# Optimization experiments

Hardware: AMD Instinct MI355X
Metric: run time of the kernel (lower is better)

Reference implementation:

```python
import jax, jax.numpy as jnp
import numpy as np
from jax import lax

EPS = 1e-5
K = 7
G = 4


def _dwconv_bn(x, w, g, b, m, v):
    # depthwise 3x3, pad 1, then BN (eval mode with running stats)
    C = x.shape[1]
    y = lax.conv_general_dilated(x, w, (1, 1), [(1, 1), (1, 1)],
                                 feature_group_count=C,
                                 dimension_numbers=('NCHW', 'OIHW', 'NCHW'))
    scale = (g / jnp.sqrt(v + EPS))[None, :, None, None]
    return (y - m[None, :, None, None]) * scale + b[None, :, None, None]


def _proj(t, pw1, pb1, pw2, pb2):
    # 1x1 conv -> GELU(exact) -> 1x1 conv, on small spatial maps
    h = jnp.einsum('bchw,oc->bohw', t, pw1) + pb1[None, :, None, None]
    h = jax.nn.gelu(h, approximate=False)
    return jnp.einsum('bchw,oc->bohw', h, pw2) + pb2[None, :, None, None]


def setup_inputs() -> dict:
    key = jax.random.key(0)
    ks = jax.random.split(key, 17)
    B, C, H, W = 16, 256, 56, 56
    r = C // 4
    inp = {
        'x1': jax.random.normal(ks[0], (B, C, H, W), jnp.float32),
        'dw1_w': jax.random.normal(ks[1], (C, 1, 3, 3), jnp.float32) * 0.1,
        'dw1_g': jax.random.uniform(ks[2], (C,), jnp.float32, 0.5, 1.5),
        'dw1_b': jax.random.normal(ks[3], (C,), jnp.float32) * 0.1,
        'dw1_m': jax.random.normal(ks[4], (C,), jnp.float32) * 0.1,
        'dw1_v': jax.random.uniform(ks[5], (C,), jnp.float32, 0.5, 1.5),
        'dw2_w': jax.random.normal(ks[6], (C, 1, 3, 3), jnp.float32) * 0.1,
        'dw2_g': jax.random.uniform(ks[7], (C,), jnp.float32, 0.5, 1.5),
        'dw2_b': jax.random.normal(ks[8], (C,), jnp.float32) * 0.1,
        'dw2_m': jax.random.normal(ks[9], (C,), jnp.float32) * 0.1,
        'dw2_v': jax.random.uniform(ks[10], (C,), jnp.float32, 0.5, 1.5),
        'weight1': jax.random.normal(ks[11], (G, C, K, K), jnp.float32) * 0.02,
        'bias1': jax.random.normal(ks[12], (G, C), jnp.float32) * 0.02,
        'pw1': jax.random.normal(ks[13], (r, C), jnp.float32) * 0.05,
        'pb1': jax.random.normal(ks[14], (r,), jnp.float32) * 0.05,
        'pw2': jax.random.normal(ks[15], (C * G, r), jnp.float32) * 0.05,
        'pb2': jax.random.normal(ks[16], (C * G,), jnp.float32) * 0.05,
    }
    return inp


def reference(x1, dw1_w, dw1_g, dw1_b, dw1_m, dw1_v,
              dw2_w, dw2_g, dw2_b, dw2_m, dw2_v,
              weight1, bias1, pw1, pb1, pw2, pb2):
    B, C, H, W = x1.shape
    # gated fuse: relu6(dw1(x)) * dw2(x)
    a = jnp.clip(_dwconv_bn(x1, dw1_w, dw1_g, dw1_b, dw1_m, dw1_v), 0.0, 6.0)
    x_fuse = a * _dwconv_bn(x1, dw2_w, dw2_g, dw2_b, dw2_m, dw2_v)

    # adaptive avg pool to (K,K): H,W multiples of K -> uniform block means
    pooled = x_fuse.reshape(B, C, K, H // K, K, W // K).mean(axis=(3, 5))

    # dynamic kernel: proj -> softmax over groups -> weighted sum of weight1
    scale1 = _proj(pooled, pw1, pb1, pw2, pb2).reshape(B, G, C, K, K)
    scale1 = jax.nn.softmax(scale1, axis=1)
    w_dyn = jnp.sum(scale1 * weight1[None], axis=1)  # [B, C, K, K]

    # dynamic bias
    mean_x = x_fuse.mean(axis=(-2, -1), keepdims=True)  # [B, C, 1, 1]
    sb = _proj(mean_x, pw1, pb1, pw2, pb2).reshape(B, G, C)
    sb = jax.nn.softmax(sb, axis=1)
    b_dyn = jnp.sum(sb * bias1[None], axis=1)  # [B, C]

    # per-sample depthwise conv with dynamic weights
    pad = K // 2

    def per_sample(xi, wi):  # xi [C,H,W], wi [C,K,K]
        y = lax.conv_general_dilated(xi[None], wi[:, None], (1, 1),
                                     [(pad, pad), (pad, pad)],
                                     feature_group_count=C,
                                     dimension_numbers=('NCHW', 'OIHW', 'NCHW'))
        return y[0]

    out = jax.vmap(per_sample)(x_fuse, w_dyn)  # [B, C, H, W]
    return out + b_dyn[:, :, None, None]
```

## Files before the change

kernel.cpp:

```cpp
#include <hip/hip_runtime.h>
#include <math.h>

#define BATCH 16
#define CH 256
#define HW 56
#define NPIX (HW*HW)

__device__ __forceinline__ void fuse_tile(
    const float* __restrict__ plane, int ty, int tx,
    const float w1[9], const float w2[9],
    float sc1, float be1, float sc2, float be2,
    float res[4][4])
{
    const int oy = 4 * ty;
    float y1a[4][4], y2a[4][4];
    #pragma unroll
    for (int a = 0; a < 4; a++)
        #pragma unroll
        for (int e = 0; e < 4; e++) { y1a[a][e] = 0.f; y2a[a][e] = 0.f; }

    #pragma unroll
    for (int iy = 0; iy < 6; iy++) {
        const int r    = oy - 1 + iy;
        const bool rok = (r >= 0) && (r < 56);
        const int rc   = rok ? r : 0;
        float rb[12];
        #pragma unroll
        for (int k = 0; k < 3; k++) {
            const int cx  = tx - 1 + k;
            const bool cv = (cx >= 0) && (cx < 14);
            const int cc2 = cv ? cx : 0;
            const bool ok = rok && cv;
            float4 v = *(const float4*)(plane + rc*56 + 4*cc2);
            rb[4*k+0] = ok ? v.x : 0.f;
            rb[4*k+1] = ok ? v.y : 0.f;
            rb[4*k+2] = ok ? v.z : 0.f;
            rb[4*k+3] = ok ? v.w : 0.f;
        }
        #pragma unroll
        for (int tyy = 0; tyy < 4; tyy++) {
            const int ky = iy - tyy;
            if (ky >= 0 && ky < 3) {
                #pragma unroll
                for (int e = 0; e < 4; e++)
                    #pragma unroll
                    for (int dj = 0; dj < 3; dj++) {
                        float xv = rb[3 + e + dj];
                        y1a[tyy][e] += xv * w1[ky*3+dj];
                        y2a[tyy][e] += xv * w2[ky*3+dj];
                    }
            }
        }
    }
    #pragma unroll
    for (int tyy = 0; tyy < 4; tyy++)
        #pragma unroll
        for (int e = 0; e < 4; e++) {
            float y1 = y1a[tyy][e] * sc1 + be1;
            float y2 = y2a[tyy][e] * sc2 + be2;
            float a = fminf(fmaxf(y1, 0.f), 6.f);
            res[tyy][e] = a * y2;
        }
}

__global__ __launch_bounds__(256) void k1_pool(
    const float* __restrict__ x1,
    const float* __restrict__ dw1w, const float* __restrict__ g1, const float* __restrict__ b1,
    const float* __restrict__ m1, const float* __restrict__ v1,
    const float* __restrict__ dw2w, const float* __restrict__ g2, const float* __restrict__ b2,
    const float* __restrict__ m2, const float* __restrict__ v2,
    float* __restrict__ pooled)
{
    const int bc = blockIdx.x;
    const int c  = bc & 255;
    const int t  = threadIdx.x;

    __shared__ float part[196];

    float w1[9], w2[9];
    #pragma unroll
    for (int k = 0; k < 9; k++) { w1[k] = dw1w[c*9+k]; w2[k] = dw2w[c*9+k]; }
    const float sc1 = g1[c] * rsqrtf(v1[c] + 1e-5f);
    const float be1 = b1[c] - m1[c] * sc1;
    const float sc2 = g2[c] * rsqrtf(v2[c] + 1e-5f);
    const float be2 = b2[c] - m2[c] * sc2;

    if (t < 196) {
        const int ty = t / 14, tx = t - ty * 14;
        float res[4][4];
        fuse_tile(x1 + (size_t)bc * NPIX, ty, tx, w1, w2, sc1, be1, sc2, be2, res);
        float s = 0.f;
        #pragma unroll
        for (int a = 0; a < 4; a++)
            #pragma unroll
            for (int e = 0; e < 4; e++) s += res[a][e];
        part[t] = s;
    }
    __syncthreads();
    if (t < 49) {
        int ph = t / 7, pw = t - ph * 7;
        float s = part[(2*ph  )*14 + 2*pw] + part[(2*ph  )*14 + 2*pw + 1]
                + part[(2*ph+1)*14 + 2*pw] + part[(2*ph+1)*14 + 2*pw + 1];
        pooled[(size_t)bc * 49 + t] = s * (1.f/64.f);
    }
}

__global__ __launch_bounds__(256) void k2a(
    const float* __restrict__ pooled, const float* __restrict__ pw1,
    const float* __restrict__ pb1, float* __restrict__ h)
{
    const int b  = blockIdx.x;
    const int oc = blockIdx.y;
    const int t  = threadIdx.x;
    __shared__ float pl[256*50];

    const float* pp = pooled + (size_t)b * 256 * 49;
    for (int idx = t; idx < 256*49; idx += 256) {
        int cc = idx / 49, p = idx - cc * 49;
        pl[cc*50 + p] = pp[idx];
    }
    __syncthreads();
    {
        float s = 0.f;
        #pragma unroll
        for (int p = 0; p < 49; p++) s += pl[t*50 + p];
        pl[t*50 + 49] = s * (1.f/49.f);
    }
    __syncthreads();

    for (int idx = t; idx < 16*50; idx += 256) {
        int ol = idx / 50, p = idx - ol * 50;
        int o = oc * 16 + ol;
        const float* wrow = pw1 + o * 256;
        float acc = pb1[o];
        #pragma unroll 8
        for (int cc = 0; cc < 256; cc++) acc += wrow[cc] * pl[cc*50 + p];
        float gv = 0.5f * acc * (1.f + erff(acc * 0.70710678118654752f));
        h[((size_t)b * 50 + p) * 64 + o] = gv;
    }
}

__global__ __launch_bounds__(256) void k2b(
    const float* __restrict__ h, const float* __restrict__ pw2, const float* __restrict__ pb2,
    const float* __restrict__ weight1, const float* __restrict__ bias1,
    float* __restrict__ w_dyn, float* __restrict__ b_dyn)
{
    const int b   = blockIdx.x;
    const int cch = blockIdx.y;
    const int t   = threadIdx.x;
    const int c_base = cch * 16;

    __shared__ __attribute__((aligned(16))) float hl[50*64];
    __shared__ float sl[64*51];

    const float* hp = h + (size_t)b * 50 * 64;
    for (int i = t; i < 800; i += 256) ((float4*)hl)[i] = ((const float4*)hp)[i];

    const int row = t & 63;
    const int pb  = t >> 6;
    const int g   = row >> 4, cl = row & 15;
    const int o2  = (g << 8) + c_base + cl;

    float wreg[64];
    {
        const float4* w4 = (const float4*)(pw2 + (size_t)o2 * 64);
        #pragma unroll
        for (int r4 = 0; r4 < 16; r4++) {
            float4 v = w4[r4];
            wreg[4*r4] = v.x; wreg[4*r4+1] = v.y; wreg[4*r4+2] = v.z; wreg[4*r4+3] = v.w;
        }
    }
    const float bias2 = pb2[o2];
    __syncthreads();

    for (int p = pb; p < 50; p += 4) {
        const float4* hv = (const float4*)&hl[p*64];
        float acc = bias2;
        #pragma unroll
        for (int r4 = 0; r4 < 16; r4++) {
            float4 v = hv[r4];
            acc += wreg[4*r4]*v.x + wreg[4*r4+1]*v.y + wreg[4*r4+2]*v.z + wreg[4*r4+3]*v.w;
        }
        sl[row*51 + p] = acc;
    }
    __syncthreads();

    for (int idx = t; idx < 16*50; idx += 256) {
        int cl2 = idx / 50, p = idx - cl2 * 50;
        float s0 = sl[(cl2     )*51 + p];
        float s1 = sl[(16 + cl2)*51 + p];
        float s2 = sl[(32 + cl2)*51 + p];
        float s3 = sl[(48 + cl2)*51 + p];
        float mx = fmaxf(fmaxf(s0, s1), fmaxf(s2, s3));
        float e0 = expf(s0-mx), e1 = expf(s1-mx), e2 = expf(s2-mx), e3 = expf(s3-mx);
        float inv = 1.f / (e0+e1+e2+e3);
        e0 *= inv; e1 *= inv; e2 *= inv; e3 *= inv;
        int cc = c_base + cl2;
        if (p < 49) {
            float wv = e0*weight1[(0*256+cc)*49+p] + e1*weight1[(1*256+cc)*49+p]
                     + e2*weight1[(2*256+cc)*49+p] + e3*weight1[(3*256+cc)*49+p];
            w_dyn[((size_t)b*256 + cc)*49 + p] = wv;
        } else {
            b_dyn[b*256 + cc] = e0*bias1[cc] + e1*bias1[256+cc] + e2*bias1[512+cc] + e3*bias1[768+cc];
        }
    }
}

#define S3 68
__global__ __launch_bounds__(256) void k3_dyn(
    const float* __restrict__ x1,
    const float* __restrict__ dw1w, const float* __restrict__ g1, const float* __restrict__ b1,
    const float* __restrict__ m1, const float* __restrict__ v1,
    const float* __restrict__ dw2w, const float* __restrict__ g2, const float* __restrict__ b2,
    const float* __restrict__ m2, const float* __restrict__ v2,
    const float* __restrict__ w_dyn, const float* __restrict__ b_dyn,
    float* __restrict__ out)
{
    const int bc = blockIdx.x;
    const int c  = bc & 255;
    const int t  = threadIdx.x;
    __shared__ __attribute__((aligned(16))) float halo[62*S3];

    float w1[9], w2[9];
    #pragma unroll
    for (int k = 0; k < 9; k++) { w1[k] = dw1w[c*9+k]; w2[k] = dw2w[c*9+k]; }
    const float sc1 = g1[c] * rsqrtf(v1[c] + 1e-5f);
    const float be1 = b1[c] - m1[c] * sc1;
    const float sc2 = g2[c] * rsqrtf(v2[c] + 1e-5f);
    const float be2 = b2[c] - m2[c] * sc2;
    float wk[49];
    const float* wp = w_dyn + (size_t)bc * 49;
    #pragma unroll
    for (int k = 0; k < 49; k++) wk[k] = wp[k];
    const float bias = b_dyn[bc];

    {
        float4 z = make_float4(0.f, 0.f, 0.f, 0.f);
        float4* h4 = (float4*)halo;
        for (int i = t; i < 62*S3/4; i += 256) h4[i] = z;
    }
    __syncthreads();

    const int ty = t / 14, tx = t - ty * 14;
    if (t < 196) {
        float res[4][4];
        fuse_tile(x1 + (size_t)bc * NPIX, ty, tx, w1, w2, sc1, be1, sc2, be2, res);
        #pragma unroll
        for (int tyy = 0; tyy < 4; tyy++) {
            float4 r4; r4.x=res[tyy][0]; r4.y=res[tyy][1]; r4.z=res[tyy][2]; r4.w=res[tyy][3];
            *(float4*)&halo[(4*ty + tyy + 3)*S3 + 4 + 4*tx] = r4;
        }
    }
    __syncthreads();

    if (t < 196) {
        const int oy = ty * 4, ox = tx * 4;
        float acc[4][4];
        #pragma unroll
        for (int a = 0; a < 4; a++)
            #pragma unroll
            for (int bb = 0; bb < 4; bb++) acc[a][bb] = bias;

        #pragma unroll
        for (int iy = 0; iy < 10; iy++) {
            const float* hr = &halo[(oy+iy)*S3 + ox];
            float4 a = *(const float4*)hr;
            float4 b = *(const float4*)(hr + 4);
            float4 cc = *(const float4*)(hr + 8);
            float row[12];
            row[0]=a.x; row[1]=a.y; row[2]=a.z; row[3]=a.w;
            row[4]=b.x; row[5]=b.y; row[6]=b.z; row[7]=b.w;
            row[8]=cc.x; row[9]=cc.y; row[10]=cc.z; row[11]=cc.w;
            #pragma unroll
            for (int tyy = 0; tyy < 4; tyy++) {
                const int ky = iy - tyy;
                if (ky >= 0 && ky < 7) {
                    #pragma unroll
                    for (int txx = 0; txx < 4; txx++)
                        #pragma unroll
                        for (int kx = 0; kx < 7; kx++)
                            acc[tyy][txx] += row[1+txx+kx] * wk[ky*7+kx];
                }
            }
        }
        float* op = out + (size_t)bc * NPIX;
        #pragma unroll
        for (int tyy = 0; tyy < 4; tyy++) {
            float4 r4; r4.x = acc[tyy][0]; r4.y = acc[tyy][1]; r4.z = acc[tyy][2]; r4.w = acc[tyy][3];
            *(float4*)(op + (oy+tyy)*56 + ox) = r4;
        }
    }
}

extern "C" void kernel_launch(void* const* d_in, const int* in_sizes, int n_in,
                              void* d_out, int out_size, void* d_ws, size_t ws_size,
                              hipStream_t stream) {
    const float* x1    = (const float*)d_in[0];
    const float* dw1w  = (const float*)d_in[1];
    const float* dw1g  = (const float*)d_in[2];
    const float* dw1b  = (const float*)d_in[3];
    const float* dw1m  = (const float*)d_in[4];
    const float* dw1v  = (const float*)d_in[5];
    const float* dw2w  = (const float*)d_in[6];
    const float* dw2g  = (const float*)d_in[7];
    const float* dw2b  = (const float*)d_in[8];
    const float* dw2m  = (const float*)d_in[9];
    const float* dw2v  = (const float*)d_in[10];
    const float* weight1 = (const float*)d_in[11];
    const float* bias1   = (const float*)d_in[12];
    const float* pw1     = (const float*)d_in[13];
    const float* pb1     = (const float*)d_in[14];
    const float* pw2     = (const float*)d_in[15];
    const float* pb2     = (const float*)d_in[16];

    float* out = (float*)d_out;
    float* ws  = (float*)d_ws;
    float* pooled = ws;
    float* h      = ws + 200704;
    float* w_dyn  = ws + 251904;
    float* b_dyn  = ws + 452608;

    k1_pool<<<BATCH*CH, 256, 0, stream>>>(x1, dw1w, dw1g, dw1b, dw1m, dw1v,
                                          dw2w, dw2g, dw2b, dw2m, dw2v, pooled);
    k2a<<<dim3(BATCH, 4), 256, 0, stream>>>(pooled, pw1, pb1, h);
    k2b<<<dim3(BATCH, 16), 256, 0, stream>>>(h, pw2, pb2, weight1, bias1, w_dyn, b_dyn);
    k3_dyn<<<BATCH*CH, 256, 0, stream>>>(x1, dw1w, dw1g, dw1b, dw1m, dw1v,
                                         dw2w, dw2g, dw2b, dw2m, dw2v,
                                         w_dyn, b_dyn, out);
}
```

Measured before the change: 202.1 us.

## Materialize padded fused activation in first kernel instead of recomputing in dynamic conv

The first kernel now stores the fused activation (two BN'd 3x3 depthwise convs combined with relu6 product) into a zero-padded 62x64 workspace plane alongside the pooled means. The dynamic 7x7 conv kernel reads that plane directly from global memory instead of recomputing the fused tile into shared memory. This removes duplicated stencil compute, shared-memory staging and barriers in the last kernel, at the cost of writing and re-reading a large intermediate tensor through HBM.

```diff
diff --git a/kernel.cpp b/kernel.cpp
--- a/kernel.cpp
+++ b/kernel.cpp
@@ -5,6 +5,9 @@
 #define CH 256
 #define HW 56
 #define NPIX (HW*HW)
+#define PR 62
+#define PS 64
+#define PPLANE (PR*PS)
 
 __device__ __forceinline__ void fuse_tile(
     const float* __restrict__ plane, int ty, int tx,
@@ -63,12 +66,13 @@
         }
 }
 
-__global__ __launch_bounds__(256) void k1_pool(
+__global__ __launch_bounds__(256) void k1_fuse(
     const float* __restrict__ x1,
     const float* __restrict__ dw1w, const float* __restrict__ g1, const float* __restrict__ b1,
     const float* __restrict__ m1, const float* __restrict__ v1,
     const float* __restrict__ dw2w, const float* __restrict__ g2, const float* __restrict__ b2,
     const float* __restrict__ m2, const float* __restrict__ v2,
+    float* __restrict__ xf,
     float* __restrict__ pooled)
 {
     const int bc = blockIdx.x;
@@ -85,9 +89,9 @@
     const float sc2 = g2[c] * rsqrtf(v2[c] + 1e-5f);
     const float be2 = b2[c] - m2[c] * sc2;
 
+    const int ty = t / 14, tx = t - ty * 14;
+    float res[4][4];
     if (t < 196) {
-        const int ty = t / 14, tx = t - ty * 14;
-        float res[4][4];
         fuse_tile(x1 + (size_t)bc * NPIX, ty, tx, w1, w2, sc1, be1, sc2, be2, res);
         float s = 0.f;
         #pragma unroll
@@ -97,11 +101,27 @@
         part[t] = s;
     }
     __syncthreads();
+
+    float* xfp = xf + (size_t)bc * PPLANE;
     if (t < 49) {
         int ph = t / 7, pw = t - ph * 7;
         float s = part[(2*ph  )*14 + 2*pw] + part[(2*ph  )*14 + 2*pw + 1]
                 + part[(2*ph+1)*14 + 2*pw] + part[(2*ph+1)*14 + 2*pw + 1];
         pooled[(size_t)bc * 49 + t] = s * (1.f/64.f);
+    }
+    if (t < 196) {
+        #pragma unroll
+        for (int tyy = 0; tyy < 4; tyy++) {
+            float4 r4; r4.x=res[tyy][0]; r4.y=res[tyy][1]; r4.z=res[tyy][2]; r4.w=res[tyy][3];
+            *(float4*)&xfp[(4*ty + tyy + 3)*PS + 4 + 4*tx] = r4;
+        }
+    }
+    if (t < 208) {
+        float4 z = make_float4(0.f, 0.f, 0.f, 0.f);
+        int prow, pc4;
+        if (t < 96) { int r = t >> 4; prow = (r < 3) ? r : (r + 56); pc4 = t & 15; }
+        else        { int t2 = t - 96; prow = 3 + (t2 >> 1); pc4 = (t2 & 1) ? 15 : 0; }
+        *(float4*)&xfp[prow*PS + 4*pc4] = z;
     }
 }
 
@@ -206,55 +226,23 @@
     }
 }
 
-#define S3 68
 __global__ __launch_bounds__(256) void k3_dyn(
-    const float* __restrict__ x1,
-    const float* __restrict__ dw1w, const float* __restrict__ g1, const float* __restrict__ b1,
-    const float* __restrict__ m1, const float* __restrict__ v1,
-    const float* __restrict__ dw2w, const float* __restrict__ g2, const float* __restrict__ b2,
-    const float* __restrict__ m2, const float* __restrict__ v2,
+    const float* __restrict__ xf,
     const float* __restrict__ w_dyn, const float* __restrict__ b_dyn,
     float* __restrict__ out)
 {
     const int bc = blockIdx.x;
-    const int c  = bc & 255;
     const int t  = threadIdx.x;
-    __shared__ __attribute__((aligned(16))) float halo[62*S3];
-
-    float w1[9], w2[9];
-    #pragma unroll
-    for (int k = 0; k < 9; k++) { w1[k] = dw1w[c*9+k]; w2[k] = dw2w[c*9+k]; }
-    const float sc1 = g1[c] * rsqrtf(v1[c] + 1e-5f);
-    const float be1 = b1[c] - m1[c] * sc1;
-    const float sc2 = g2[c] * rsqrtf(v2[c] + 1e-5f);
-    const float be2 = b2[c] - m2[c] * sc2;
+
     float wk[49];
     const float* wp = w_dyn + (size_t)bc * 49;
     #pragma unroll
     for (int k = 0; k < 49; k++) wk[k] = wp[k];
     const float bias = b_dyn[bc];
 
-    {
-        float4 z = make_float4(0.f, 0.f, 0.f, 0.f);
-        float4* h4 = (float4*)halo;
-        for (int i = t; i < 62*S3/4; i += 256) h4[i] = z;
-    }
-    __syncthreads();
-
-    const int ty = t / 14, tx = t - ty * 14;
     if (t < 196) {
-        float res[4][4];
-        fuse_tile(x1 + (size_t)bc * NPIX, ty, tx, w1, w2, sc1, be1, sc2, be2, res);
-        #pragma unroll
-        for (int tyy = 0; tyy < 4; tyy++) {
-            float4 r4; r4.x=res[tyy][0]; r4.y=res[tyy][1]; r4.z=res[tyy][2]; r4.w=res[tyy][3];
-            *(float4*)&halo[(4*ty + tyy + 3)*S3 + 4 + 4*tx] = r4;
-        }
-    }
-    __syncthreads();
-
-    if (t < 196) {
-        const int oy = ty * 4, ox = tx * 4;
+        const int ty = t / 14, tx = t - ty * 14;
+        const float* xfp = xf + (size_t)bc * PPLANE + 4*tx;
         float acc[4][4];
         #pragma unroll
         for (int a = 0; a < 4; a++)
@@ -263,14 +251,14 @@
 
         #pragma unroll
         for (int iy = 0; iy < 10; iy++) {
-            const float* hr = &halo[(oy+iy)*S3 + ox];
+            const float* hr = xfp + (4*ty + iy) * PS;
             float4 a = *(const float4*)hr;
             float4 b = *(const float4*)(hr + 4);
-            float4 cc = *(const float4*)(hr + 8);
+            float4 c = *(const float4*)(hr + 8);
             float row[12];
             row[0]=a.x; row[1]=a.y; row[2]=a.z; row[3]=a.w;
             row[4]=b.x; row[5]=b.y; row[6]=b.z; row[7]=b.w;
-            row[8]=cc.x; row[9]=cc.y; row[10]=cc.z; row[11]=cc.w;
+            row[8]=c.x; row[9]=c.y; row[10]=c.z; row[11]=c.w;
             #pragma unroll
             for (int tyy = 0; tyy < 4; tyy++) {
                 const int ky = iy - tyy;
@@ -287,7 +275,7 @@
         #pragma unroll
         for (int tyy = 0; tyy < 4; tyy++) {
             float4 r4; r4.x = acc[tyy][0]; r4.y = acc[tyy][1]; r4.z = acc[tyy][2]; r4.w = acc[tyy][3];
-            *(float4*)(op + (oy+tyy)*56 + ox) = r4;
+            *(float4*)(op + (4*ty+tyy)*56 + 4*tx) = r4;
         }
     }
 }
@@ -315,16 +303,15 @@
 
     float* out = (float*)d_out;
     float* ws  = (float*)d_ws;
-    float* pooled = ws;
-    float* h      = ws + 200704;
-    float* w_dyn  = ws + 251904;
-    float* b_dyn  = ws + 452608;
-
-    k1_pool<<<BATCH*CH, 256, 0, stream>>>(x1, dw1w, dw1g, dw1b, dw1m, dw1v,
-                                          dw2w, dw2g, dw2b, dw2m, dw2v, pooled);
+    float* xfuse  = ws;
+    float* pooled = ws + 16252928;
+    float* h      = ws + 16453632;
+    float* w_dyn  = ws + 16504832;
+    float* b_dyn  = ws + 16705536;
+
+    k1_fuse<<<BATCH*CH, 256, 0, stream>>>(x1, dw1w, dw1g, dw1b, dw1m, dw1v,
+                                          dw2w, dw2g, dw2b, dw2m, dw2v, xfuse, pooled);
     k2a<<<dim3(BATCH, 4), 256, 0, stream>>>(pooled, pw1, pb1, h);
     k2b<<<dim3(BATCH, 16), 256, 0, stream>>>(h, pw2, pb2, weight1, bias1, w_dyn, b_dyn);
-    k3_dyn<<<BATCH*CH, 256, 0, stream>>>(x1, dw1w, dw1g, dw1b, dw1m, dw1v,
-                                         dw2w, dw2g, dw2b, dw2m, dw2v,
-                                         w_dyn, b_dyn, out);
-}
+    k3_dyn<<<BATCH*CH, 256, 0, stream>>>(xfuse, w_dyn, b_dyn, out);
+}
```

After: 207.5 us. +2.7%, slower.
